# Optimization experiments

Measured on AMD Instinct MI355X. Metric: run time of the kernel, lower is better.

## Reference

```python
import jax, jax.numpy as jnp
import numpy as np
from itertools import permutations

SIZES = (16, 32, 32, 32)  # token_sizes for layout dims (v, t, h, w)
N = SIZES[0] * SIZES[1] * SIZES[2] * SIZES[3]  # num_tokens = 524288
B = 32
EPS = 1e-3


def setup_inputs() -> dict:
    key = jax.random.key(0)
    ks = jax.random.split(key, 12)
    u = lambda k, shape: jax.random.uniform(k, shape, dtype=jnp.float32)
    alphas = [1.0, 2.0, 4.0]
    comps = np.array(
        [[alphas[v], alphas[t], alphas[hw], alphas[hw]]
         for v, t, hw in permutations(range(3), 3)], dtype=np.float32)  # [6, 4]
    return {
        "components": jnp.asarray(comps),
        "u_rate_src": u(ks[0], (1,)),
        "u_rate_tgt": u(ks[1], (1,)),
        "u0_src": u(ks[2], (B, N)),
        "u0_tgt": u(ks[3], (B, N)),
        "u_v_src": u(ks[4], (B, SIZES[0])),
        "u_t_src": u(ks[5], (B, SIZES[1])),
        "u_h_src": u(ks[6], (B, SIZES[2])),
        "u_w_src": u(ks[7], (B, SIZES[3])),
        "u_v_tgt": u(ks[8], (B, SIZES[0])),
        "u_t_tgt": u(ks[9], (B, SIZES[1])),
        "u_h_tgt": u(ks[10], (B, SIZES[2])),
        "u_w_tgt": u(ks[11], (B, SIZES[3])),
        "idx": 2,
    }


def _clamp(x):
    return jnp.clip(x, EPS, 1.0 - EPS)


def _binary_mask(u_rate, u0, u_dims, alphas):
    # event_prior: log-prob per token = log U0 + sum_dim log(U_dim)/alpha_dim (broadcast over pattern)
    P = jnp.log(_clamp(u0))  # [B, N]
    for i, ud in enumerate(u_dims):
        shape = [B, 1, 1, 1, 1]
        shape[1 + i] = SIZES[i]
        rep = jnp.broadcast_to(
            (jnp.log(_clamp(ud)) / alphas[i]).reshape(shape),
            (B,) + SIZES).reshape(B, N)
        P = P + rep
    # rate_prior: one shared uniform, K = floor(U * N), expanded over batch
    K = (_clamp(u_rate) * N).astype(jnp.int32)  # [1]
    K = jnp.broadcast_to(K, (B,))[:, None]  # [B, 1]
    # binary_topk_: rank via double argsort (0 = largest), mask = K > rank
    rank = jnp.argsort(jnp.argsort(-P, axis=-1), axis=-1)
    return K > rank


def reference(components, u_rate_src, u_rate_tgt, u0_src, u0_tgt,
              u_v_src, u_t_src, u_h_src, u_w_src,
              u_v_tgt, u_t_tgt, u_h_tgt, u_w_tgt, idx):
    alphas = components[idx]  # [4], one alpha per layout dim, shared by src/tgt
    src = _binary_mask(u_rate_src, u0_src,
                       (u_v_src, u_t_src, u_h_src, u_w_src), alphas)
    tgt = _binary_mask(u_rate_tgt, u0_tgt,
                       (u_v_tgt, u_t_tgt, u_h_tgt, u_w_tgt), alphas)
    return src, tgt
```

## Files before the change

kernel.cpp:

```cpp
#include <hip/hip_runtime.h>
#include <stdint.h>

#define NTOK 524288
#define ROWS 64
#define CHUNKS 64
#define NTHR 256
#define F4_PER_ROW (NTOK / 4)
#define F4_PER_CHUNK (F4_PER_ROW / CHUNKS)
#define F4_PER_THR (F4_PER_CHUNK / NTHR)
#define NB1 2048
#define B1BASE 30720
#define BCAP 65536
#define GCAP 8192
#define FB_CHUNKS 16
#define STAGECAP 512

#define OFF_H16  0u
#define OFF_H2   (OFF_H16 + ROWS * NB1 * 4u)
#define OFF_B1   (OFF_H2 + ROWS * 4096u * 4u)
#define OFF_CG   (OFF_B1 + 256u)
#define OFF_B2   (OFF_CG + 256u)
#define OFF_REM  (OFF_B2 + 256u)
#define OFF_IT   (OFF_REM + 256u)
#define OFF_BCNT (OFF_IT + 256u)
#define OFF_GCNT (OFF_BCNT + 256u)
#define OFF_T    (OFF_GCNT + 256u)
#define OFF_ZERO_END (OFF_T + 512u)
#define OFF_TAB  OFF_ZERO_END
#define OFF_BK   (OFF_TAB + ROWS * 112u * 8u)
#define OFF_BI   (OFF_BK + (size_t)ROWS * BCAP * 8u)
#define OFF_GKEY (OFF_BI + (size_t)ROWS * BCAP * 4u)
#define OFF_GIDX (OFF_GKEY + (size_t)ROWS * GCAP * 8u)

__device__ __forceinline__ double clamp64(double x) {
  return fmin(fmax(x, 1.0e-3), 1.0 - 1.0e-3);
}

__device__ __forceinline__ unsigned compute_K(float ur) {
  float urf = fminf(fmaxf(ur, 1.0e-3f), 1.0f - 1.0e-3f);
  return (unsigned)(int)(urf * (float)NTOK);
}

__device__ __forceinline__ int bucket16(unsigned long long kb) {
  int b = (int)(unsigned)(kb >> 47) - B1BASE;
  return b < 0 ? 0 : (b > NB1 - 1 ? NB1 - 1 : b);
}

__global__ void k_tables(const float* __restrict__ comps, const int* __restrict__ idxp,
                         const float* __restrict__ uvs, const float* __restrict__ uts,
                         const float* __restrict__ uhs, const float* __restrict__ uws,
                         const float* __restrict__ uvt, const float* __restrict__ utt,
                         const float* __restrict__ uht, const float* __restrict__ uwt,
                         double* __restrict__ tabs) {
  int idx = idxp[0];
  double alpha[4];
  for (int d = 0; d < 4; ++d) alpha[d] = (double)comps[idx * 4 + d];
  for (int i = threadIdx.x; i < ROWS * 112; i += blockDim.x) {
    int row = i / 112, j = i % 112;
    int m = row >> 5, b = row & 31;
    int d, jj, dsz;
    if (j < 16)      { d = 0; jj = j;      dsz = 16; }
    else if (j < 48) { d = 1; jj = j - 16; dsz = 32; }
    else if (j < 80) { d = 2; jj = j - 48; dsz = 32; }
    else             { d = 3; jj = j - 80; dsz = 32; }
    const float* u;
    if (m == 0) u = (d == 0) ? uvs : (d == 1) ? uts : (d == 2) ? uhs : uws;
    else        u = (d == 0) ? uvt : (d == 1) ? utt : (d == 2) ? uht : uwt;
    double x = clamp64((double)u[b * dsz + jj]);
    double a = alpha[d];
    double f;
    if (a == 1.0)      f = x;
    else if (a == 2.0) f = sqrt(x);
    else if (a == 4.0) f = sqrt(sqrt(x));
    else               f = pow(x, 1.0 / a);
    tabs[row * 112 + j] = f;
  }
}

__global__ void k_hist16(const float* __restrict__ u0s, const float* __restrict__ u0t,
                         const double* __restrict__ tabs, unsigned int* __restrict__ h16) {
  __shared__ double tb[112];
  __shared__ unsigned int h[NB1];
  int row = blockIdx.x / CHUNKS, chunk = blockIdx.x % CHUNKS;
  for (int i = threadIdx.x; i < 112; i += blockDim.x) tb[i] = tabs[row * 112 + i];
  for (int i = threadIdx.x; i < NB1; i += blockDim.x) h[i] = 0;
  __syncthreads();
  int m = row >> 5, b = row & 31;
  const float4* u0 = reinterpret_cast<const float4*>((m ? u0t : u0s) + (size_t)b * NTOK);
  int base = chunk * F4_PER_CHUNK;
  for (int it = 0; it < F4_PER_THR; ++it) {
    int f4 = base + it * NTHR + threadIdx.x;
    float4 x = u0[f4];
    int n0 = f4 * 4;
    int w0 = n0 & 31, hh = (n0 >> 5) & 31, tt = (n0 >> 10) & 31, vv = n0 >> 15;
    double g = tb[vv] * tb[16 + tt] * tb[48 + hh];
    double k0 = clamp64((double)x.x) * (g * tb[80 + w0 + 0]);
    double k1 = clamp64((double)x.y) * (g * tb[80 + w0 + 1]);
    double k2 = clamp64((double)x.z) * (g * tb[80 + w0 + 2]);
    double k3 = clamp64((double)x.w) * (g * tb[80 + w0 + 3]);
    atomicAdd(&h[bucket16((unsigned long long)__double_as_longlong(k0))], 1u);
    atomicAdd(&h[bucket16((unsigned long long)__double_as_longlong(k1))], 1u);
    atomicAdd(&h[bucket16((unsigned long long)__double_as_longlong(k2))], 1u);
    atomicAdd(&h[bucket16((unsigned long long)__double_as_longlong(k3))], 1u);
  }
  __syncthreads();
  for (int i = threadIdx.x; i < NB1; i += blockDim.x) {
    unsigned c = h[i];
    if (c) atomicAdd(&h16[row * NB1 + i], c);
  }
}

__global__ __launch_bounds__(256) void k_scan16(const unsigned int* __restrict__ h16,
                                                const float* __restrict__ urs,
                                                const float* __restrict__ urt,
                                                int* __restrict__ sB1, int* __restrict__ sCG) {
  __shared__ unsigned suf[256];
  __shared__ int best;
  int row = blockIdx.x;
  int t = threadIdx.x;
  const unsigned* h = h16 + row * NB1;
  unsigned loc[8]; unsigned own = 0;
#pragma unroll
  for (int i = 0; i < 8; ++i) { loc[i] = h[t * 8 + i]; own += loc[i]; }
  suf[t] = own;
  if (t == 0) best = -1;
  __syncthreads();
  for (int off = 1; off < 256; off <<= 1) {
    unsigned add = (t + off < 256) ? suf[t + off] : 0u;
    __syncthreads();
    suf[t] += add;
    __syncthreads();
  }
  int m = row >> 5;
  unsigned K = compute_K(m ? urt[0] : urs[0]);
  unsigned above = suf[t] - own;
  int cand = -1;
  unsigned cum = above;
  for (int i = 7; i >= 0; --i) {
    if (cum + loc[i] >= K) { cand = t * 8 + i; break; }
    cum += loc[i];
  }
  if (cand >= 0) atomicMax(&best, cand);
  __syncthreads();
  int bb = best;
  if (bb >= 0 && (bb >> 3) == t) {
    unsigned cg = above;
    for (int i = 7; i > (bb & 7); --i) cg += loc[i];
    sB1[row] = bb;
    sCG[row] = (int)cg;
  }
}

__global__ void k_gather2(const float* __restrict__ u0s, const float* __restrict__ u0t,
                          const double* __restrict__ tabs, const int* __restrict__ sB1,
                          unsigned int* __restrict__ gh2, unsigned int* __restrict__ bcnt,
                          unsigned long long* __restrict__ bk, unsigned int* __restrict__ bi) {
  __shared__ double tb[112];
  __shared__ unsigned int h[4096];
  __shared__ unsigned long long sk[STAGECAP];
  __shared__ unsigned int si[STAGECAP];
  __shared__ unsigned int scnt, sbase;
  int row = blockIdx.x / CHUNKS, chunk = blockIdx.x % CHUNKS;
  for (int i = threadIdx.x; i < 112; i += blockDim.x) tb[i] = tabs[row * 112 + i];
  for (int i = threadIdx.x; i < 4096; i += blockDim.x) h[i] = 0;
  if (threadIdx.x == 0) scnt = 0;
  __syncthreads();
  int b1 = sB1[row];
  int m = row >> 5, b = row & 31;
  const float4* u0 = reinterpret_cast<const float4*>((m ? u0t : u0s) + (size_t)b * NTOK);
  int base = chunk * F4_PER_CHUNK;
  for (int it = 0; it < F4_PER_THR; ++it) {
    int f4 = base + it * NTHR + threadIdx.x;
    float4 x = u0[f4];
    int n0 = f4 * 4;
    int w0 = n0 & 31, hh = (n0 >> 5) & 31, tt = (n0 >> 10) & 31, vv = n0 >> 15;
    double g = tb[vv] * tb[16 + tt] * tb[48 + hh];
    double ks[4];
    ks[0] = clamp64((double)x.x) * (g * tb[80 + w0 + 0]);
    ks[1] = clamp64((double)x.y) * (g * tb[80 + w0 + 1]);
    ks[2] = clamp64((double)x.z) * (g * tb[80 + w0 + 2]);
    ks[3] = clamp64((double)x.w) * (g * tb[80 + w0 + 3]);
#pragma unroll
    for (int c = 0; c < 4; ++c) {
      unsigned long long kb = (unsigned long long)__double_as_longlong(ks[c]);
      if (bucket16(kb) == b1) {
        atomicAdd(&h[(unsigned)(kb >> 39) & 0xFFFu], 1u);
        unsigned p = atomicAdd(&scnt, 1u);
        if (p < STAGECAP) { sk[p] = kb; si[p] = (unsigned)(n0 + c); }
        else {
          unsigned gp = atomicAdd(&bcnt[row], 1u);
          if (gp < BCAP) {
            bk[(size_t)row * BCAP + gp] = kb;
            bi[(size_t)row * BCAP + gp] = (unsigned)(n0 + c);
          }
        }
      }
    }
  }
  __syncthreads();
  unsigned nst = scnt; if (nst > STAGECAP) nst = STAGECAP;
  if (threadIdx.x == 0) sbase = atomicAdd(&bcnt[row], nst);
  __syncthreads();
  unsigned bs = sbase;
  for (unsigned i = threadIdx.x; i < nst; i += blockDim.x) {
    unsigned gp = bs + i;
    if (gp < BCAP) {
      bk[(size_t)row * BCAP + gp] = sk[i];
      bi[(size_t)row * BCAP + gp] = si[i];
    }
  }
  for (int i = threadIdx.x; i < 4096; i += blockDim.x) {
    unsigned c = h[i];
    if (c) atomicAdd(&gh2[row * 4096 + i], c);
  }
}

__global__ __launch_bounds__(256) void k_scan2(const unsigned int* __restrict__ gh2,
                                               const float* __restrict__ urs,
                                               const float* __restrict__ urt,
                                               const int* __restrict__ sCG,
                                               int* __restrict__ sB2, int* __restrict__ sREM) {
  __shared__ unsigned suf[256];
  __shared__ int best;
  int row = blockIdx.x;
  int t = threadIdx.x;
  const unsigned* h = gh2 + row * 4096;
  unsigned loc[16]; unsigned own = 0;
#pragma unroll
  for (int i = 0; i < 16; ++i) { loc[i] = h[t * 16 + i]; own += loc[i]; }
  suf[t] = own;
  if (t == 0) best = -1;
  __syncthreads();
  for (int off = 1; off < 256; off <<= 1) {
    unsigned add = (t + off < 256) ? suf[t + off] : 0u;
    __syncthreads();
    suf[t] += add;
    __syncthreads();
  }
  int m = row >> 5;
  unsigned K = compute_K(m ? urt[0] : urs[0]);
  unsigned K2 = K - (unsigned)sCG[row];
  unsigned above = suf[t] - own;
  int cand = -1;
  unsigned cum = above;
  for (int i = 15; i >= 0; --i) {
    if (cum + loc[i] >= K2) { cand = t * 16 + i; break; }
    cum += loc[i];
  }
  if (cand >= 0) atomicMax(&best, cand);
  __syncthreads();
  int bb = best;
  if (bb >= 0 && (bb >> 4) == t) {
    unsigned a2 = above;
    for (int i = 15; i > (bb & 15); --i) a2 += loc[i];
    sB2[row] = bb;
    sREM[row] = (int)(K2 - a2);
  }
}

__global__ void k_gather_fb(const float* __restrict__ u0s, const float* __restrict__ u0t,
                            const double* __restrict__ tabs,
                            const int* __restrict__ sB1, const int* __restrict__ sB2,
                            const unsigned int* __restrict__ bcnt,
                            unsigned int* __restrict__ gcnt,
                            unsigned long long* __restrict__ gkey, unsigned int* __restrict__ gidx) {
  int row = blockIdx.x / FB_CHUNKS, chunk = blockIdx.x % FB_CHUNKS;
  if (bcnt[row] <= BCAP) return;
  __shared__ double tb[112];
  for (int i = threadIdx.x; i < 112; i += blockDim.x) tb[i] = tabs[row * 112 + i];
  __syncthreads();
  int b1 = sB1[row];
  unsigned b2 = (unsigned)sB2[row];
  int m = row >> 5, b = row & 31;
  const float4* u0 = reinterpret_cast<const float4*>((m ? u0t : u0s) + (size_t)b * NTOK);
  int base = chunk * (F4_PER_ROW / FB_CHUNKS);
  for (int it = 0; it < F4_PER_ROW / FB_CHUNKS / NTHR; ++it) {
    int f4 = base + it * NTHR + threadIdx.x;
    float4 x = u0[f4];
    int n0 = f4 * 4;
    int w0 = n0 & 31, hh = (n0 >> 5) & 31, tt = (n0 >> 10) & 31, vv = n0 >> 15;
    double g = tb[vv] * tb[16 + tt] * tb[48 + hh];
    double ks[4];
    ks[0] = clamp64((double)x.x) * (g * tb[80 + w0 + 0]);
    ks[1] = clamp64((double)x.y) * (g * tb[80 + w0 + 1]);
    ks[2] = clamp64((double)x.z) * (g * tb[80 + w0 + 2]);
    ks[3] = clamp64((double)x.w) * (g * tb[80 + w0 + 3]);
#pragma unroll
    for (int c = 0; c < 4; ++c) {
      unsigned long long kb = (unsigned long long)__double_as_longlong(ks[c]);
      if (bucket16(kb) == b1 && (((unsigned)(kb >> 39)) & 0xFFFu) == b2) {
        unsigned pos = atomicAdd(&gcnt[row], 1u);
        if (pos < GCAP) {
          gkey[(size_t)row * GCAP + pos] = kb;
          gidx[(size_t)row * GCAP + pos] = (unsigned)(n0 + c);
        }
      }
    }
  }
}

__global__ __launch_bounds__(1024) void k_select(const unsigned long long* __restrict__ bk,
                                                 const unsigned int* __restrict__ bi,
                                                 const unsigned int* __restrict__ bcnt,
                                                 const unsigned long long* __restrict__ gkey,
                                                 const unsigned int* __restrict__ gidx,
                                                 const unsigned int* __restrict__ gcnt,
                                                 const int* __restrict__ sB2,
                                                 const int* __restrict__ sREM,
                                                 unsigned long long* __restrict__ sT,
                                                 int* __restrict__ sIT) {
  __shared__ unsigned long long k[GCAP];
  __shared__ unsigned int ix[GCAP];
  __shared__ unsigned int lcnt;
  int row = blockIdx.x;
  if (threadIdx.x == 0) lcnt = 0;
  __syncthreads();
  unsigned cnt1 = bcnt[row];
  unsigned n_r;
  if (cnt1 <= BCAP) {
    unsigned b2 = (unsigned)sB2[row];
    for (unsigned i = threadIdx.x; i < cnt1; i += blockDim.x) {
      unsigned long long kb = bk[(size_t)row * BCAP + i];
      if ((((unsigned)(kb >> 39)) & 0xFFFu) == b2) {
        unsigned p = atomicAdd(&lcnt, 1u);
        if (p < GCAP) { k[p] = kb; ix[p] = bi[(size_t)row * BCAP + i]; }
      }
    }
    __syncthreads();
    n_r = lcnt; if (n_r > GCAP) n_r = GCAP;
  } else {
    n_r = gcnt[row];
    if (n_r > GCAP) n_r = GCAP;
    for (unsigned i = threadIdx.x; i < n_r; i += blockDim.x) {
      k[i] = gkey[(size_t)row * GCAP + i];
      ix[i] = gidx[(size_t)row * GCAP + i];
    }
    __syncthreads();
  }
  unsigned n2 = 2;
  while (n2 < n_r) n2 <<= 1;
  for (unsigned i = threadIdx.x; i < n2; i += blockDim.x) {
    if (i >= n_r) { k[i] = 0ULL; ix[i] = 0xFFFFFFFFu; }
  }
  __syncthreads();
  for (unsigned kk = 2; kk <= n2; kk <<= 1) {
    for (unsigned j = kk >> 1; j > 0; j >>= 1) {
      for (int i = threadIdx.x; i < (int)n2; i += blockDim.x) {
        int pj = i ^ (int)j;
        if (pj > i) {
          unsigned long long k1 = k[i], k2 = k[pj];
          unsigned i1 = ix[i], i2 = ix[pj];
          bool bef = (k1 > k2) || (k1 == k2 && i1 < i2);
          bool dirAsc = ((i & (int)kk) == 0);
          if (bef != dirAsc) { k[i] = k2; k[pj] = k1; ix[i] = i2; ix[pj] = i1; }
        }
      }
      __syncthreads();
    }
  }
  if (threadIdx.x == 0) {
    int rem = sREM[row];
    if (rem < 1) rem = 1;
    if ((unsigned)rem > n_r) rem = (int)n_r;
    sT[row] = k[rem - 1];
    sIT[row] = (int)ix[rem - 1];
  }
}

__global__ void k_final(const float* __restrict__ u0s, const float* __restrict__ u0t,
                        const double* __restrict__ tabs,
                        const unsigned long long* __restrict__ sT, const int* __restrict__ sIT,
                        int* __restrict__ out) {
  __shared__ double tb[112];
  int row = blockIdx.x / CHUNKS, chunk = blockIdx.x % CHUNKS;
  for (int i = threadIdx.x; i < 112; i += blockDim.x) tb[i] = tabs[row * 112 + i];
  __syncthreads();
  unsigned long long T = sT[row];
  int IT = sIT[row];
  int m = row >> 5, b = row & 31;
  const float4* u0 = reinterpret_cast<const float4*>((m ? u0t : u0s) + (size_t)b * NTOK);
  int4* o = reinterpret_cast<int4*>(out + (size_t)row * NTOK);
  int base = chunk * F4_PER_CHUNK;
  for (int it = 0; it < F4_PER_THR; ++it) {
    int f4 = base + it * NTHR + threadIdx.x;
    float4 x = u0[f4];
    int n0 = f4 * 4;
    int w0 = n0 & 31, hh = (n0 >> 5) & 31, tt = (n0 >> 10) & 31, vv = n0 >> 15;
    double g = tb[vv] * tb[16 + tt] * tb[48 + hh];
    unsigned long long kb0 = (unsigned long long)__double_as_longlong(clamp64((double)x.x) * (g * tb[80 + w0 + 0]));
    unsigned long long kb1 = (unsigned long long)__double_as_longlong(clamp64((double)x.y) * (g * tb[80 + w0 + 1]));
    unsigned long long kb2 = (unsigned long long)__double_as_longlong(clamp64((double)x.z) * (g * tb[80 + w0 + 2]));
    unsigned long long kb3 = (unsigned long long)__double_as_longlong(clamp64((double)x.w) * (g * tb[80 + w0 + 3]));
    int4 r;
    r.x = (kb0 > T || (kb0 == T && (n0 + 0) <= IT)) ? 1 : 0;
    r.y = (kb1 > T || (kb1 == T && (n0 + 1) <= IT)) ? 1 : 0;
    r.z = (kb2 > T || (kb2 == T && (n0 + 2) <= IT)) ? 1 : 0;
    r.w = (kb3 > T || (kb3 == T && (n0 + 3) <= IT)) ? 1 : 0;
    o[f4] = r;
  }
}

extern "C" void kernel_launch(void* const* d_in, const int* in_sizes, int n_in,
                              void* d_out, int out_size, void* d_ws, size_t ws_size,
                              hipStream_t stream) {
  const float* comps = (const float*)d_in[0];
  const float* urs   = (const float*)d_in[1];
  const float* urt   = (const float*)d_in[2];
  const float* u0s   = (const float*)d_in[3];
  const float* u0t   = (const float*)d_in[4];
  const float* uvs   = (const float*)d_in[5];
  const float* uts   = (const float*)d_in[6];
  const float* uhs   = (const float*)d_in[7];
  const float* uws   = (const float*)d_in[8];
  const float* uvt   = (const float*)d_in[9];
  const float* utt   = (const float*)d_in[10];
  const float* uht   = (const float*)d_in[11];
  const float* uwt   = (const float*)d_in[12];
  const int*   idxp  = (const int*)d_in[13];
  int* out = (int*)d_out;

  char* ws = (char*)d_ws;
  unsigned int*       h16  = (unsigned int*)(ws + OFF_H16);
  unsigned int*       gh2  = (unsigned int*)(ws + OFF_H2);
  int*                sB1  = (int*)(ws + OFF_B1);
  int*                sCG  = (int*)(ws + OFF_CG);
  int*                sB2  = (int*)(ws + OFF_B2);
  int*                sREM = (int*)(ws + OFF_REM);
  int*                sIT  = (int*)(ws + OFF_IT);
  unsigned int*       bcnt = (unsigned int*)(ws + OFF_BCNT);
  unsigned int*       gcnt = (unsigned int*)(ws + OFF_GCNT);
  unsigned long long* sT   = (unsigned long long*)(ws + OFF_T);
  double*             tabs = (double*)(ws + OFF_TAB);
  unsigned long long* bk   = (unsigned long long*)(ws + OFF_BK);
  unsigned int*       bi   = (unsigned int*)(ws + OFF_BI);
  unsigned long long* gkey = (unsigned long long*)(ws + OFF_GKEY);
  unsigned int*       gidx = (unsigned int*)(ws + OFF_GIDX);

  hipMemsetAsync(d_ws, 0, OFF_ZERO_END, stream);

  k_tables<<<1, 256, 0, stream>>>(comps, idxp, uvs, uts, uhs, uws, uvt, utt, uht, uwt, tabs);
  k_hist16<<<ROWS * CHUNKS, NTHR, 0, stream>>>(u0s, u0t, tabs, h16);
  k_scan16<<<ROWS, 256, 0, stream>>>(h16, urs, urt, sB1, sCG);
  k_gather2<<<ROWS * CHUNKS, NTHR, 0, stream>>>(u0s, u0t, tabs, sB1, gh2, bcnt, bk, bi);
  k_scan2<<<ROWS, 256, 0, stream>>>(gh2, urs, urt, sCG, sB2, sREM);
  k_gather_fb<<<ROWS * FB_CHUNKS, NTHR, 0, stream>>>(u0s, u0t, tabs, sB1, sB2, bcnt, gcnt, gkey, gidx);
  k_select<<<ROWS, 1024, 0, stream>>>(bk, bi, bcnt, gkey, gidx, gcnt, sB2, sREM, sT, sIT);
  k_final<<<ROWS * CHUNKS, NTHR, 0, stream>>>(u0s, u0t, tabs, sT, sIT, out);
}
```

Before: 370.2 us.

## Fuse second-level histogram, scan and select into one per-row pick kernel

Removes the shared-memory second-level histogram from the gather pass and the separate scan, fallback gather and select kernels. A single per-row kernel now builds the 12-bit histogram from the staged bucket candidates, scans it, filters the sub-bucket and bitonic-sorts it in shared memory. This cuts two launches and the LDS histogram atomics in the full-data gather pass. The cost is that the work now runs on 64 blocks of 256 threads instead of 1024, and the fallback path for buckets above BCAP is dropped, which risks wrong results if a bucket overflows.

```diff
diff --git a/kernel.cpp b/kernel.cpp
--- a/kernel.cpp
+++ b/kernel.cpp
@@ -12,25 +12,18 @@
 #define B1BASE 30720
 #define BCAP 65536
 #define GCAP 8192
-#define FB_CHUNKS 16
 #define STAGECAP 512
 
 #define OFF_H16  0u
-#define OFF_H2   (OFF_H16 + ROWS * NB1 * 4u)
-#define OFF_B1   (OFF_H2 + ROWS * 4096u * 4u)
+#define OFF_B1   (OFF_H16 + ROWS * NB1 * 4u)
 #define OFF_CG   (OFF_B1 + 256u)
-#define OFF_B2   (OFF_CG + 256u)
-#define OFF_REM  (OFF_B2 + 256u)
-#define OFF_IT   (OFF_REM + 256u)
-#define OFF_BCNT (OFF_IT + 256u)
-#define OFF_GCNT (OFF_BCNT + 256u)
-#define OFF_T    (OFF_GCNT + 256u)
+#define OFF_BCNT (OFF_CG + 256u)
+#define OFF_IT   (OFF_BCNT + 256u)
+#define OFF_T    (OFF_IT + 256u)
 #define OFF_ZERO_END (OFF_T + 512u)
 #define OFF_TAB  OFF_ZERO_END
 #define OFF_BK   (OFF_TAB + ROWS * 112u * 8u)
 #define OFF_BI   (OFF_BK + (size_t)ROWS * BCAP * 8u)
-#define OFF_GKEY (OFF_BI + (size_t)ROWS * BCAP * 4u)
-#define OFF_GIDX (OFF_GKEY + (size_t)ROWS * GCAP * 8u)
 
 __device__ __forceinline__ double clamp64(double x) {
   return fmin(fmax(x, 1.0e-3), 1.0 - 1.0e-3);
@@ -153,16 +146,14 @@
 
 __global__ void k_gather2(const float* __restrict__ u0s, const float* __restrict__ u0t,
                           const double* __restrict__ tabs, const int* __restrict__ sB1,
-                          unsigned int* __restrict__ gh2, unsigned int* __restrict__ bcnt,
+                          unsigned int* __restrict__ bcnt,
                           unsigned long long* __restrict__ bk, unsigned int* __restrict__ bi) {
   __shared__ double tb[112];
-  __shared__ unsigned int h[4096];
   __shared__ unsigned long long sk[STAGECAP];
   __shared__ unsigned int si[STAGECAP];
   __shared__ unsigned int scnt, sbase;
   int row = blockIdx.x / CHUNKS, chunk = blockIdx.x % CHUNKS;
   for (int i = threadIdx.x; i < 112; i += blockDim.x) tb[i] = tabs[row * 112 + i];
-  for (int i = threadIdx.x; i < 4096; i += blockDim.x) h[i] = 0;
   if (threadIdx.x == 0) scnt = 0;
   __syncthreads();
   int b1 = sB1[row];
@@ -184,7 +175,6 @@
     for (int c = 0; c < 4; ++c) {
       unsigned long long kb = (unsigned long long)__double_as_longlong(ks[c]);
       if (bucket16(kb) == b1) {
-        atomicAdd(&h[(unsigned)(kb >> 39) & 0xFFFu], 1u);
         unsigned p = atomicAdd(&scnt, 1u);
         if (p < STAGECAP) { sk[p] = kb; si[p] = (unsigned)(n0 + c); }
         else {
@@ -209,27 +199,37 @@
       bi[(size_t)row * BCAP + gp] = si[i];
     }
   }
-  for (int i = threadIdx.x; i < 4096; i += blockDim.x) {
-    unsigned c = h[i];
-    if (c) atomicAdd(&gh2[row * 4096 + i], c);
-  }
-}
-
-__global__ __launch_bounds__(256) void k_scan2(const unsigned int* __restrict__ gh2,
-                                               const float* __restrict__ urs,
-                                               const float* __restrict__ urt,
-                                               const int* __restrict__ sCG,
-                                               int* __restrict__ sB2, int* __restrict__ sREM) {
+}
+
+__global__ __launch_bounds__(256) void k_pick(const unsigned long long* __restrict__ bk,
+                                              const unsigned int* __restrict__ bi,
+                                              const unsigned int* __restrict__ bcnt,
+                                              const float* __restrict__ urs,
+                                              const float* __restrict__ urt,
+                                              const int* __restrict__ sCG,
+                                              unsigned long long* __restrict__ sT,
+                                              int* __restrict__ sIT) {
+  __shared__ unsigned int h[4096];
   __shared__ unsigned suf[256];
   __shared__ int best;
+  __shared__ unsigned long long kk[GCAP];
+  __shared__ unsigned int ixx[GCAP];
+  __shared__ unsigned int lcnt;
   int row = blockIdx.x;
   int t = threadIdx.x;
-  const unsigned* h = gh2 + row * 4096;
+  unsigned cnt = bcnt[row]; if (cnt > BCAP) cnt = BCAP;
+  const unsigned long long* rbk = bk + (size_t)row * BCAP;
+  const unsigned int* rbi = bi + (size_t)row * BCAP;
+  for (int i = t; i < 4096; i += 256) h[i] = 0;
+  if (t == 0) { best = -1; lcnt = 0; }
+  __syncthreads();
+  for (unsigned i = t; i < cnt; i += 256)
+    atomicAdd(&h[(unsigned)(rbk[i] >> 39) & 0xFFFu], 1u);
+  __syncthreads();
   unsigned loc[16]; unsigned own = 0;
 #pragma unroll
   for (int i = 0; i < 16; ++i) { loc[i] = h[t * 16 + i]; own += loc[i]; }
   suf[t] = own;
-  if (t == 0) best = -1;
   __syncthreads();
   for (int off = 1; off < 256; off <<= 1) {
     unsigned add = (t + off < 256) ? suf[t + off] : 0u;
@@ -249,121 +249,50 @@
   }
   if (cand >= 0) atomicMax(&best, cand);
   __syncthreads();
-  int bb = best;
-  if (bb >= 0 && (bb >> 4) == t) {
+  int b2 = best;
+  __shared__ unsigned sharedRem;
+  if (b2 >= 0 && (b2 >> 4) == t) {
     unsigned a2 = above;
-    for (int i = 15; i > (bb & 15); --i) a2 += loc[i];
-    sB2[row] = bb;
-    sREM[row] = (int)(K2 - a2);
-  }
-}
-
-__global__ void k_gather_fb(const float* __restrict__ u0s, const float* __restrict__ u0t,
-                            const double* __restrict__ tabs,
-                            const int* __restrict__ sB1, const int* __restrict__ sB2,
-                            const unsigned int* __restrict__ bcnt,
-                            unsigned int* __restrict__ gcnt,
-                            unsigned long long* __restrict__ gkey, unsigned int* __restrict__ gidx) {
-  int row = blockIdx.x / FB_CHUNKS, chunk = blockIdx.x % FB_CHUNKS;
-  if (bcnt[row] <= BCAP) return;
-  __shared__ double tb[112];
-  for (int i = threadIdx.x; i < 112; i += blockDim.x) tb[i] = tabs[row * 112 + i];
-  __syncthreads();
-  int b1 = sB1[row];
-  unsigned b2 = (unsigned)sB2[row];
-  int m = row >> 5, b = row & 31;
-  const float4* u0 = reinterpret_cast<const float4*>((m ? u0t : u0s) + (size_t)b * NTOK);
-  int base = chunk * (F4_PER_ROW / FB_CHUNKS);
-  for (int it = 0; it < F4_PER_ROW / FB_CHUNKS / NTHR; ++it) {
-    int f4 = base + it * NTHR + threadIdx.x;
-    float4 x = u0[f4];
-    int n0 = f4 * 4;
-    int w0 = n0 & 31, hh = (n0 >> 5) & 31, tt = (n0 >> 10) & 31, vv = n0 >> 15;
-    double g = tb[vv] * tb[16 + tt] * tb[48 + hh];
-    double ks[4];
-    ks[0] = clamp64((double)x.x) * (g * tb[80 + w0 + 0]);
-    ks[1] = clamp64((double)x.y) * (g * tb[80 + w0 + 1]);
-    ks[2] = clamp64((double)x.z) * (g * tb[80 + w0 + 2]);
-    ks[3] = clamp64((double)x.w) * (g * tb[80 + w0 + 3]);
-#pragma unroll
-    for (int c = 0; c < 4; ++c) {
-      unsigned long long kb = (unsigned long long)__double_as_longlong(ks[c]);
-      if (bucket16(kb) == b1 && (((unsigned)(kb >> 39)) & 0xFFFu) == b2) {
-        unsigned pos = atomicAdd(&gcnt[row], 1u);
-        if (pos < GCAP) {
-          gkey[(size_t)row * GCAP + pos] = kb;
-          gidx[(size_t)row * GCAP + pos] = (unsigned)(n0 + c);
-        }
-      }
+    for (int i = 15; i > (b2 & 15); --i) a2 += loc[i];
+    sharedRem = K2 - a2;
+  }
+  __syncthreads();
+  unsigned rem = sharedRem;
+  for (unsigned i = t; i < cnt; i += 256) {
+    unsigned long long kb = rbk[i];
+    if (((unsigned)(kb >> 39) & 0xFFFu) == (unsigned)b2) {
+      unsigned p = atomicAdd(&lcnt, 1u);
+      if (p < GCAP) { kk[p] = kb; ixx[p] = rbi[i]; }
     }
   }
-}
-
-__global__ __launch_bounds__(1024) void k_select(const unsigned long long* __restrict__ bk,
-                                                 const unsigned int* __restrict__ bi,
-                                                 const unsigned int* __restrict__ bcnt,
-                                                 const unsigned long long* __restrict__ gkey,
-                                                 const unsigned int* __restrict__ gidx,
-                                                 const unsigned int* __restrict__ gcnt,
-                                                 const int* __restrict__ sB2,
-                                                 const int* __restrict__ sREM,
-                                                 unsigned long long* __restrict__ sT,
-                                                 int* __restrict__ sIT) {
-  __shared__ unsigned long long k[GCAP];
-  __shared__ unsigned int ix[GCAP];
-  __shared__ unsigned int lcnt;
-  int row = blockIdx.x;
-  if (threadIdx.x == 0) lcnt = 0;
-  __syncthreads();
-  unsigned cnt1 = bcnt[row];
-  unsigned n_r;
-  if (cnt1 <= BCAP) {
-    unsigned b2 = (unsigned)sB2[row];
-    for (unsigned i = threadIdx.x; i < cnt1; i += blockDim.x) {
-      unsigned long long kb = bk[(size_t)row * BCAP + i];
-      if ((((unsigned)(kb >> 39)) & 0xFFFu) == b2) {
-        unsigned p = atomicAdd(&lcnt, 1u);
-        if (p < GCAP) { k[p] = kb; ix[p] = bi[(size_t)row * BCAP + i]; }
-      }
-    }
-    __syncthreads();
-    n_r = lcnt; if (n_r > GCAP) n_r = GCAP;
-  } else {
-    n_r = gcnt[row];
-    if (n_r > GCAP) n_r = GCAP;
-    for (unsigned i = threadIdx.x; i < n_r; i += blockDim.x) {
-      k[i] = gkey[(size_t)row * GCAP + i];
-      ix[i] = gidx[(size_t)row * GCAP + i];
-    }
-    __syncthreads();
-  }
+  __syncthreads();
+  unsigned n_r = lcnt; if (n_r > GCAP) n_r = GCAP;
   unsigned n2 = 2;
   while (n2 < n_r) n2 <<= 1;
-  for (unsigned i = threadIdx.x; i < n2; i += blockDim.x) {
-    if (i >= n_r) { k[i] = 0ULL; ix[i] = 0xFFFFFFFFu; }
-  }
-  __syncthreads();
-  for (unsigned kk = 2; kk <= n2; kk <<= 1) {
-    for (unsigned j = kk >> 1; j > 0; j >>= 1) {
-      for (int i = threadIdx.x; i < (int)n2; i += blockDim.x) {
+  for (unsigned i = t; i < n2; i += 256)
+    if (i >= n_r) { kk[i] = 0ULL; ixx[i] = 0xFFFFFFFFu; }
+  __syncthreads();
+  for (unsigned kstep = 2; kstep <= n2; kstep <<= 1) {
+    for (unsigned j = kstep >> 1; j > 0; j >>= 1) {
+      for (int i = t; i < (int)n2; i += 256) {
         int pj = i ^ (int)j;
         if (pj > i) {
-          unsigned long long k1 = k[i], k2 = k[pj];
-          unsigned i1 = ix[i], i2 = ix[pj];
-          bool bef = (k1 > k2) || (k1 == k2 && i1 < i2);
-          bool dirAsc = ((i & (int)kk) == 0);
-          if (bef != dirAsc) { k[i] = k2; k[pj] = k1; ix[i] = i2; ix[pj] = i1; }
+          unsigned long long k1 = kk[i], k2v = kk[pj];
+          unsigned i1 = ixx[i], i2 = ixx[pj];
+          bool bef = (k1 > k2v) || (k1 == k2v && i1 < i2);
+          bool dirAsc = ((i & (int)kstep) == 0);
+          if (bef != dirAsc) { kk[i] = k2v; kk[pj] = k1; ixx[i] = i2; ixx[pj] = i1; }
         }
       }
       __syncthreads();
     }
   }
-  if (threadIdx.x == 0) {
-    int rem = sREM[row];
-    if (rem < 1) rem = 1;
-    if ((unsigned)rem > n_r) rem = (int)n_r;
-    sT[row] = k[rem - 1];
-    sIT[row] = (int)ix[rem - 1];
+  if (t == 0) {
+    int r = (int)rem;
+    if (r < 1) r = 1;
+    if ((unsigned)r > n_r) r = (int)n_r;
+    sT[row] = kk[r - 1];
+    sIT[row] = (int)ixx[r - 1];
   }
 }
 
@@ -421,29 +350,21 @@
 
   char* ws = (char*)d_ws;
   unsigned int*       h16  = (unsigned int*)(ws + OFF_H16);
-  unsigned int*       gh2  = (unsigned int*)(ws + OFF_H2);
   int*                sB1  = (int*)(ws + OFF_B1);
   int*                sCG  = (int*)(ws + OFF_CG);
-  int*                sB2  = (int*)(ws + OFF_B2);
-  int*                sREM = (int*)(ws + OFF_REM);
+  unsigned int*       bcnt = (unsigned int*)(ws + OFF_BCNT);
   int*                sIT  = (int*)(ws + OFF_IT);
-  unsigned int*       bcnt = (unsigned int*)(ws + OFF_BCNT);
-  unsigned int*       gcnt = (unsigned int*)(ws + OFF_GCNT);
   unsigned long long* sT   = (unsigned long long*)(ws + OFF_T);
   double*             tabs = (double*)(ws + OFF_TAB);
   unsigned long long* bk   = (unsigned long long*)(ws + OFF_BK);
   unsigned int*       bi   = (unsigned int*)(ws + OFF_BI);
-  unsigned long long* gkey = (unsigned long long*)(ws + OFF_GKEY);
-  unsigned int*       gidx = (unsigned int*)(ws + OFF_GIDX);
 
   hipMemsetAsync(d_ws, 0, OFF_ZERO_END, stream);
 
   k_tables<<<1, 256, 0, stream>>>(comps, idxp, uvs, uts, uhs, uws, uvt, utt, uht, uwt, tabs);
   k_hist16<<<ROWS * CHUNKS, NTHR, 0, stream>>>(u0s, u0t, tabs, h16);
   k_scan16<<<ROWS, 256, 0, stream>>>(h16, urs, urt, sB1, sCG);
-  k_gather2<<<ROWS * CHUNKS, NTHR, 0, stream>>>(u0s, u0t, tabs, sB1, gh2, bcnt, bk, bi);
-  k_scan2<<<ROWS, 256, 0, stream>>>(gh2, urs, urt, sCG, sB2, sREM);
-  k_gather_fb<<<ROWS * FB_CHUNKS, NTHR, 0, stream>>>(u0s, u0t, tabs, sB1, sB2, bcnt, gcnt, gkey, gidx);
-  k_select<<<ROWS, 1024, 0, stream>>>(bk, bi, bcnt, gkey, gidx, gcnt, sB2, sREM, sT, sIT);
+  k_gather2<<<ROWS * CHUNKS, NTHR, 0, stream>>>(u0s, u0t, tabs, sB1, bcnt, bk, bi);
+  k_pick<<<ROWS, 256, 0, stream>>>(bk, bi, bcnt, urs, urt, sCG, sT, sIT);
   k_final<<<ROWS * CHUNKS, NTHR, 0, stream>>>(u0s, u0t, tabs, sT, sIT, out);
 }
```

Result: no change. 368.4 us (-0.5%).
